# Performance work log

Measured on AMD Instinct MI355X. Metric: run time of the kernel, lower is better.

## Reference

```python
import jax, jax.numpy as jnp
import numpy as np
import math

ALPHA = 2.0  # spikingjelly surrogate.ATan default alpha
NB_STEPS, NUM_IN, NUM_HID, NUM_OUT = 100, 784, 100, 10
BATCH = 1024
TAU_LIF = 2.0

@jax.custom_vjp
def atan_spike(x):
    # Heaviside forward, ATan surrogate backward
    return (x >= 0.0).astype(x.dtype)

def _atan_fwd(x):
    return atan_spike(x), x

def _atan_bwd(x, g):
    return (g * (ALPHA / 2.0) / (1.0 + (jnp.pi / 2.0 * ALPHA * x) ** 2),)

atan_spike.defvjp(_atan_fwd, _atan_bwd)


def setup_inputs() -> dict:
    key = jax.random.key(0)
    ks = jax.random.split(key, 3)
    x = jax.random.normal(ks[0], (BATCH, NB_STEPS, NUM_IN), jnp.float32)
    tau_syn = 2.0
    # spikingjelly SynapseFilter(learnable=True): w init = -log(tau - 1)
    w_syn1 = jnp.asarray(-math.log(tau_syn - 1.0), jnp.float32)
    w_syn2 = jnp.asarray(-math.log(tau_syn - 1.0), jnp.float32)
    W1 = jax.random.normal(ks[1], (NUM_HID, NUM_IN), jnp.float32) / np.sqrt(NUM_IN).astype(np.float32)
    b1 = jnp.zeros((NUM_HID,), jnp.float32)
    W2 = jax.random.normal(ks[2], (NUM_OUT, NUM_HID), jnp.float32) / np.sqrt(NUM_HID).astype(np.float32)
    b2 = jnp.zeros((NUM_OUT,), jnp.float32)
    return dict(x=x, w_syn1=w_syn1, W1=W1, b1=b1, w_syn2=w_syn2, W2=W2, b2=b2)


def reference(x, w_syn1, W1, b1, w_syn2, W2, b2):
    B = x.shape[0]
    inv1 = jax.nn.sigmoid(w_syn1)  # 1/tau of filter 1
    inv2 = jax.nn.sigmoid(w_syn2)
    s1 = jnp.zeros((B, NUM_IN), x.dtype)
    v1 = jnp.zeros((B, NUM_HID), x.dtype)
    s2 = jnp.zeros((B, NUM_HID), x.dtype)
    v2 = jnp.zeros((B, NUM_OUT), x.dtype)

    def step(carry, xt):
        s1, v1, s2, v2 = carry
        # SynapseFilter 1: s = s - s*sigmoid(w) + in
        s1 = s1 - s1 * inv1 + xt
        h1 = s1 @ W1.T + b1
        # LIF 1: decay_input=True, v_reset=0: v += (x - (v - 0)) / tau
        v1 = v1 + (h1 - v1) / TAU_LIF
        sp1 = atan_spike(v1 - 1.0)       # v_threshold = 1.0
        v1 = v1 * (1.0 - sp1)            # hard reset to v_reset = 0
        # SynapseFilter 2
        s2 = s2 - s2 * inv2 + sp1
        h2 = s2 @ W2.T + b2
        # LIF 2: v_reset=None (soft reset), v_threshold=0, decay_input=True
        v2 = v2 + (h2 - v2) / TAU_LIF
        sp2 = atan_spike(v2 - 0.0)
        v2 = v2 - sp2 * 0.0              # soft reset subtracts spike*threshold (=0)
        return (s1, v1, s2, v2), None

    (s1, v1, s2, v2), _ = jax.lax.scan(step, (s1, v1, s2, v2), jnp.swapaxes(x, 0, 1))
    # Net.forward returns self.fc[-1].v: final membrane potential of last LIF
    return v2
```

## Files before the change

kernel.cpp:

```cpp
#include <hip/hip_runtime.h>
#include <math.h>


#define NSTEPS 100
#define NHID 100
#define KDIM 784
#define BK 16
#define NOUT 10

__global__ __launch_bounds__(256, 2)
void snn_fused2(const float* __restrict__ X, const float* __restrict__ wsyn1p,
                const float* __restrict__ W1, const float* __restrict__ b1,
                const float* __restrict__ wsyn2p, const float* __restrict__ W2,
                const float* __restrict__ b2, float* __restrict__ out) {
  __shared__ float Xs[BK][256];
  __shared__ float Ws[BK][112];
  __shared__ float Cs[2][25][106];
  __shared__ float zsh[2][NHID];

  const int tid = threadIdx.x;
  const int l   = tid & 63;
  const int cg  = __builtin_amdgcn_readfirstlane(tid >> 6);
  const long b0 = 2L * blockIdx.x;

  const int sb = tid >> 7;
  const int st = ((tid & 127) < NSTEPS) ? (tid & 127) : (NSTEPS - 1);
  const float* __restrict__ Xrow = X + ((b0 + sb) * NSTEPS + st) * (size_t)KDIM;
  const int wj0 = tid >> 2, wkq = tid & 3;
  const int g0 = wj0 / 25, c0 = wj0 % 25;
  const int wj1 = wj0 + 64;
  const int g1 = wj1 / 25, c1 = wj1 % 25;
  const float* __restrict__ Wp0 = W1 + (size_t)wj0 * KDIM + 4 * wkq;
  const float* __restrict__ Wp1 = W1 + (size_t)wj1 * KDIM + 4 * wkq;

  float acc[4][25];
#pragma unroll
  for (int i = 0; i < 4; ++i)
#pragma unroll
    for (int c = 0; c < 25; ++c) acc[i][c] = 0.0f;

  float4 xr0 = *(const float4*)(Xrow + 0);
  float4 xr1 = *(const float4*)(Xrow + 4);
  float4 xr2 = *(const float4*)(Xrow + 8);
  float4 xr3 = *(const float4*)(Xrow + 12);
  float4 wr0 = *(const float4*)(Wp0);
  float4 wr1 = (tid < 144) ? *(const float4*)(Wp1) : float4{0, 0, 0, 0};

  for (int kt = 0; kt < KDIM; kt += BK) {
    __syncthreads();
    Xs[0][tid] = xr0.x;  Xs[1][tid] = xr0.y;  Xs[2][tid] = xr0.z;  Xs[3][tid] = xr0.w;
    Xs[4][tid] = xr1.x;  Xs[5][tid] = xr1.y;  Xs[6][tid] = xr1.z;  Xs[7][tid] = xr1.w;
    Xs[8][tid] = xr2.x;  Xs[9][tid] = xr2.y;  Xs[10][tid] = xr2.z; Xs[11][tid] = xr2.w;
    Xs[12][tid] = xr3.x; Xs[13][tid] = xr3.y; Xs[14][tid] = xr3.z; Xs[15][tid] = xr3.w;
    {
      float* w = &Ws[4 * wkq][28 * g0 + c0];
      w[0] = wr0.x; w[112] = wr0.y; w[224] = wr0.z; w[336] = wr0.w;
    }
    if (tid < 144) {
      float* w = &Ws[4 * wkq][28 * g1 + c1];
      w[0] = wr1.x; w[112] = wr1.y; w[224] = wr1.z; w[336] = wr1.w;
    }
    __syncthreads();
    if (kt + BK < KDIM) {
      const float* xp = Xrow + kt + BK;
      xr0 = *(const float4*)(xp + 0);
      xr1 = *(const float4*)(xp + 4);
      xr2 = *(const float4*)(xp + 8);
      xr3 = *(const float4*)(xp + 12);
      wr0 = *(const float4*)(Wp0 + kt + BK);
      if (tid < 144) wr1 = *(const float4*)(Wp1 + kt + BK);
    }
#pragma unroll
    for (int k = 0; k < BK; ++k) {
      const float4 xv = *(const float4*)&Xs[k][4 * l];
      const float* __restrict__ wk = &Ws[k][28 * cg];
#pragma unroll
      for (int g = 0; g < 6; ++g) {
        const float4 wv = *(const float4*)(wk + 4 * g);
        acc[0][4*g+0] = fmaf(xv.x, wv.x, acc[0][4*g+0]);
        acc[1][4*g+0] = fmaf(xv.y, wv.x, acc[1][4*g+0]);
        acc[2][4*g+0] = fmaf(xv.z, wv.x, acc[2][4*g+0]);
        acc[3][4*g+0] = fmaf(xv.w, wv.x, acc[3][4*g+0]);
        acc[0][4*g+1] = fmaf(xv.x, wv.y, acc[0][4*g+1]);
        acc[1][4*g+1] = fmaf(xv.y, wv.y, acc[1][4*g+1]);
        acc[2][4*g+1] = fmaf(xv.z, wv.y, acc[2][4*g+1]);
        acc[3][4*g+1] = fmaf(xv.w, wv.y, acc[3][4*g+1]);
        acc[0][4*g+2] = fmaf(xv.x, wv.z, acc[0][4*g+2]);
        acc[1][4*g+2] = fmaf(xv.y, wv.z, acc[1][4*g+2]);
        acc[2][4*g+2] = fmaf(xv.z, wv.z, acc[2][4*g+2]);
        acc[3][4*g+2] = fmaf(xv.w, wv.z, acc[3][4*g+2]);
        acc[0][4*g+3] = fmaf(xv.x, wv.w, acc[0][4*g+3]);
        acc[1][4*g+3] = fmaf(xv.y, wv.w, acc[1][4*g+3]);
        acc[2][4*g+3] = fmaf(xv.z, wv.w, acc[2][4*g+3]);
        acc[3][4*g+3] = fmaf(xv.w, wv.w, acc[3][4*g+3]);
      }
      const float w24 = wk[24];
      acc[0][24] = fmaf(xv.x, w24, acc[0][24]);
      acc[1][24] = fmaf(xv.y, w24, acc[1][24]);
      acc[2][24] = fmaf(xv.z, w24, acc[2][24]);
      acc[3][24] = fmaf(xv.w, w24, acc[3][24]);
    }
  }

  const float inv1 = 1.f / (1.f + expf(-wsyn1p[0]));
  const float inv2 = 1.f / (1.f + expf(-wsyn2p[0]));
  const int sb2 = tid >> 7;
  const int j   = tid & 127;
  const float bj = (j < NHID) ? b1[j] : 0.f;
  float S = 0.f, v1 = 0.f, s2 = 0.f, z = 0.f;
  float at = 0x1p-100f;

  for (int q = 0; q < 4; ++q) {
    __syncthreads();
#pragma unroll
    for (int i = 0; i < 4; ++i) {
      const int r = 4 * l + i;
      const int bb = r >> 7;
      const int t  = r & 127;
      const int tt = t - 25 * q;
      if (t < NSTEPS && tt >= 0 && tt < 25) {
#pragma unroll
        for (int c = 0; c < 25; ++c) Cs[bb][tt][25 * cg + c] = acc[i][c];
      }
    }
    __syncthreads();
    if (j < NHID) {
#pragma unroll
      for (int tt = 0; tt < 25; ++tt) {
        const float u = Cs[sb2][tt][j];
        S = S - S * inv1 + u;
        const float h = S + bj;
        v1 = v1 + (h - v1) * 0.5f;
        const float sp = (v1 >= 1.0f) ? 1.0f : 0.0f;
        v1 = v1 * (1.0f - sp);
        s2 = s2 - s2 * inv2 + sp;
        z  = fmaf(at, s2, z);
        at *= 2.0f;
      }
    }
  }

  if (j < NHID) zsh[sb2][j] = z;
  __syncthreads();

  if (tid < 2 * NOUT) {
    const int bb = tid / NOUT;
    const int jo = tid % NOUT;
    float a = b2[jo];
    const float* __restrict__ wrow = W2 + jo * NHID;
#pragma unroll
    for (int jj = 0; jj < NHID; ++jj) a = fmaf(zsh[bb][jj], wrow[jj], a);
    out[(b0 + bb) * NOUT + jo] = a;
  }
}

extern "C" void kernel_launch(void* const* d_in, const int* in_sizes, int n_in,
                              void* d_out, int out_size, void* d_ws, size_t ws_size,
                              hipStream_t stream) {
  const float* x     = (const float*)d_in[0];
  const float* wsyn1 = (const float*)d_in[1];
  const float* W1    = (const float*)d_in[2];
  const float* b1    = (const float*)d_in[3];
  const float* wsyn2 = (const float*)d_in[4];
  const float* W2    = (const float*)d_in[5];
  const float* b2    = (const float*)d_in[6];
  float* out = (float*)d_out;

  snn_fused2<<<dim3(512), dim3(256), 0, stream>>>(x, wsyn1, W1, b1, wsyn2, W2,
                                                  b2, out);
}
```

Baseline: 561.7 us.

## Pre-transpose W1 to workspace and use packed FP32 FMAs with global W reads

Adds a small kernel that transposes W1 into a padded k-major layout in the workspace. The main kernel then stops staging W through LDS and instead has each wavefront read its 25-column W slice straight from global/L2 (uniform across lanes). The inner product switches to 2-wide packed FMAs (v_pk_fma_f32) and uses a larger K tile of 28. The goal is to cut LDS traffic and barriers and to double FMA throughput, at the cost of an extra kernel launch and many per-k global loads of W that depend on cache hits.

New measurement: 554.1 us. No clear change (-1.4%).

```diff
diff --git a/kernel.cpp b/kernel.cpp
--- a/kernel.cpp
+++ b/kernel.cpp
@@ -5,16 +5,26 @@
 #define NSTEPS 100
 #define NHID 100
 #define KDIM 784
-#define BK 16
+#define BKT 28
 #define NOUT 10
 
+typedef float v2f __attribute__((ext_vector_type(2)));
+
+__global__ __launch_bounds__(256)
+void wt_transpose(const float* __restrict__ W1, float* __restrict__ Wt) {
+  const int idx = blockIdx.x * 256 + threadIdx.x;
+  if (idx >= KDIM * 128) return;
+  const int k = idx >> 7, s = idx & 127, cg = s >> 5, i = s & 31;
+  const int j = 25 * cg + i;
+  Wt[idx] = (i < 25) ? W1[(size_t)j * KDIM + k] : 0.0f;
+}
+
 __global__ __launch_bounds__(256, 2)
-void snn_fused2(const float* __restrict__ X, const float* __restrict__ wsyn1p,
-                const float* __restrict__ W1, const float* __restrict__ b1,
+void snn_fused3(const float* __restrict__ X, const float* __restrict__ Wt,
+                const float* __restrict__ wsyn1p, const float* __restrict__ b1,
                 const float* __restrict__ wsyn2p, const float* __restrict__ W2,
                 const float* __restrict__ b2, float* __restrict__ out) {
-  __shared__ float Xs[BK][256];
-  __shared__ float Ws[BK][112];
+  __shared__ float Xs[BKT][256];
   __shared__ float Cs[2][25][106];
   __shared__ float zsh[2][NHID];
 
@@ -26,79 +36,64 @@
   const int sb = tid >> 7;
   const int st = ((tid & 127) < NSTEPS) ? (tid & 127) : (NSTEPS - 1);
   const float* __restrict__ Xrow = X + ((b0 + sb) * NSTEPS + st) * (size_t)KDIM;
-  const int wj0 = tid >> 2, wkq = tid & 3;
-  const int g0 = wj0 / 25, c0 = wj0 % 25;
-  const int wj1 = wj0 + 64;
-  const int g1 = wj1 / 25, c1 = wj1 % 25;
-  const float* __restrict__ Wp0 = W1 + (size_t)wj0 * KDIM + 4 * wkq;
-  const float* __restrict__ Wp1 = W1 + (size_t)wj1 * KDIM + 4 * wkq;
 
-  float acc[4][25];
+  v2f  acc2[4][12];
+  float accs[4];
 #pragma unroll
-  for (int i = 0; i < 4; ++i)
+  for (int i = 0; i < 4; ++i) {
+    accs[i] = 0.0f;
 #pragma unroll
-    for (int c = 0; c < 25; ++c) acc[i][c] = 0.0f;
+    for (int c = 0; c < 12; ++c) acc2[i][c] = (v2f){0.0f, 0.0f};
+  }
 
-  float4 xr0 = *(const float4*)(Xrow + 0);
-  float4 xr1 = *(const float4*)(Xrow + 4);
-  float4 xr2 = *(const float4*)(Xrow + 8);
-  float4 xr3 = *(const float4*)(Xrow + 12);
-  float4 wr0 = *(const float4*)(Wp0);
-  float4 wr1 = (tid < 144) ? *(const float4*)(Wp1) : float4{0, 0, 0, 0};
+  float4 pf[7];
+#pragma unroll
+  for (int q = 0; q < 7; ++q) pf[q] = *(const float4*)(Xrow + 4 * q);
 
-  for (int kt = 0; kt < KDIM; kt += BK) {
+  const float* __restrict__ wgrp = Wt + 32 * cg;
+
+  for (int kt = 0; kt < KDIM; kt += BKT) {
     __syncthreads();
-    Xs[0][tid] = xr0.x;  Xs[1][tid] = xr0.y;  Xs[2][tid] = xr0.z;  Xs[3][tid] = xr0.w;
-    Xs[4][tid] = xr1.x;  Xs[5][tid] = xr1.y;  Xs[6][tid] = xr1.z;  Xs[7][tid] = xr1.w;
-    Xs[8][tid] = xr2.x;  Xs[9][tid] = xr2.y;  Xs[10][tid] = xr2.z; Xs[11][tid] = xr2.w;
-    Xs[12][tid] = xr3.x; Xs[13][tid] = xr3.y; Xs[14][tid] = xr3.z; Xs[15][tid] = xr3.w;
-    {
-      float* w = &Ws[4 * wkq][28 * g0 + c0];
-      w[0] = wr0.x; w[112] = wr0.y; w[224] = wr0.z; w[336] = wr0.w;
-    }
-    if (tid < 144) {
-      float* w = &Ws[4 * wkq][28 * g1 + c1];
-      w[0] = wr1.x; w[112] = wr1.y; w[224] = wr1.z; w[336] = wr1.w;
+#pragma unroll
+    for (int q = 0; q < 7; ++q) {
+      Xs[4 * q + 0][tid] = pf[q].x;
+      Xs[4 * q + 1][tid] = pf[q].y;
+      Xs[4 * q + 2][tid] = pf[q].z;
+      Xs[4 * q + 3][tid] = pf[q].w;
     }
     __syncthreads();
-    if (kt + BK < KDIM) {
-      const float* xp = Xrow + kt + BK;
-      xr0 = *(const float4*)(xp + 0);
-      xr1 = *(const float4*)(xp + 4);
-      xr2 = *(const float4*)(xp + 8);
-      xr3 = *(const float4*)(xp + 12);
-      wr0 = *(const float4*)(Wp0 + kt + BK);
-      if (tid < 144) wr1 = *(const float4*)(Wp1 + kt + BK);
+    if (kt + BKT < KDIM) {
+      const float* xp = Xrow + kt + BKT;
+#pragma unroll
+      for (int q = 0; q < 7; ++q) pf[q] = *(const float4*)(xp + 4 * q);
     }
+
+#pragma unroll 4
+    for (int k = 0; k < BKT; ++k) {
+      const float4 xv = *(const float4*)&Xs[k][4 * l];
+      const float* __restrict__ wk = wgrp + (size_t)(kt + k) * 128;
+      float w[26];
 #pragma unroll
-    for (int k = 0; k < BK; ++k) {
-      const float4 xv = *(const float4*)&Xs[k][4 * l];
-      const float* __restrict__ wk = &Ws[k][28 * cg];
+      for (int i2 = 0; i2 < 13; ++i2)
+        *(v2f*)(w + 2 * i2) = *(const v2f*)(wk + 2 * i2);
+
+      const v2f xd0 = {xv.x, xv.x};
+      const v2f xd1 = {xv.y, xv.y};
+      const v2f xd2 = {xv.z, xv.z};
+      const v2f xd3 = {xv.w, xv.w};
 #pragma unroll
-      for (int g = 0; g < 6; ++g) {
-        const float4 wv = *(const float4*)(wk + 4 * g);
-        acc[0][4*g+0] = fmaf(xv.x, wv.x, acc[0][4*g+0]);
-        acc[1][4*g+0] = fmaf(xv.y, wv.x, acc[1][4*g+0]);
-        acc[2][4*g+0] = fmaf(xv.z, wv.x, acc[2][4*g+0]);
-        acc[3][4*g+0] = fmaf(xv.w, wv.x, acc[3][4*g+0]);
-        acc[0][4*g+1] = fmaf(xv.x, wv.y, acc[0][4*g+1]);
-        acc[1][4*g+1] = fmaf(xv.y, wv.y, acc[1][4*g+1]);
-        acc[2][4*g+1] = fmaf(xv.z, wv.y, acc[2][4*g+1]);
-        acc[3][4*g+1] = fmaf(xv.w, wv.y, acc[3][4*g+1]);
-        acc[0][4*g+2] = fmaf(xv.x, wv.z, acc[0][4*g+2]);
-        acc[1][4*g+2] = fmaf(xv.y, wv.z, acc[1][4*g+2]);
-        acc[2][4*g+2] = fmaf(xv.z, wv.z, acc[2][4*g+2]);
-        acc[3][4*g+2] = fmaf(xv.w, wv.z, acc[3][4*g+2]);
-        acc[0][4*g+3] = fmaf(xv.x, wv.w, acc[0][4*g+3]);
-        acc[1][4*g+3] = fmaf(xv.y, wv.w, acc[1][4*g+3]);
-        acc[2][4*g+3] = fmaf(xv.z, wv.w, acc[2][4*g+3]);
-        acc[3][4*g+3] = fmaf(xv.w, wv.w, acc[3][4*g+3]);
+      for (int c2 = 0; c2 < 12; ++c2) {
+        const v2f wv = *(const v2f*)(w + 2 * c2);
+        acc2[0][c2] = __builtin_elementwise_fma(xd0, wv, acc2[0][c2]);
+        acc2[1][c2] = __builtin_elementwise_fma(xd1, wv, acc2[1][c2]);
+        acc2[2][c2] = __builtin_elementwise_fma(xd2, wv, acc2[2][c2]);
+        acc2[3][c2] = __builtin_elementwise_fma(xd3, wv, acc2[3][c2]);
       }
-      const float w24 = wk[24];
-      acc[0][24] = fmaf(xv.x, w24, acc[0][24]);
-      acc[1][24] = fmaf(xv.y, w24, acc[1][24]);
-      acc[2][24] = fmaf(xv.z, w24, acc[2][24]);
-      acc[3][24] = fmaf(xv.w, w24, acc[3][24]);
+      const float w24 = w[24];
+      accs[0] = fmaf(xv.x, w24, accs[0]);
+      accs[1] = fmaf(xv.y, w24, accs[1]);
+      accs[2] = fmaf(xv.z, w24, accs[2]);
+      accs[3] = fmaf(xv.w, w24, accs[3]);
     }
   }
 
@@ -114,13 +109,18 @@
     __syncthreads();
 #pragma unroll
     for (int i = 0; i < 4; ++i) {
-      const int r = 4 * l + i;
+      const int r  = 4 * l + i;
       const int bb = r >> 7;
       const int t  = r & 127;
       const int tt = t - 25 * q;
       if (t < NSTEPS && tt >= 0 && tt < 25) {
+        float* crow = &Cs[bb][tt][25 * cg];
 #pragma unroll
-        for (int c = 0; c < 25; ++c) Cs[bb][tt][25 * cg + c] = acc[i][c];
+        for (int c2 = 0; c2 < 12; ++c2) {
+          crow[2 * c2 + 0] = acc2[i][c2].x;
+          crow[2 * c2 + 1] = acc2[i][c2].y;
+        }
+        crow[24] = accs[i];
       }
     }
     __syncthreads();
@@ -165,7 +165,9 @@
   const float* W2    = (const float*)d_in[5];
   const float* b2    = (const float*)d_in[6];
   float* out = (float*)d_out;
+  float* Wt  = (float*)d_ws;
 
-  snn_fused2<<<dim3(512), dim3(256), 0, stream>>>(x, wsyn1, W1, b1, wsyn2, W2,
+  wt_transpose<<<dim3((KDIM * 128 + 255) / 256), dim3(256), 0, stream>>>(W1, Wt);
+  snn_fused3<<<dim3(512), dim3(256), 0, stream>>>(x, Wt, wsyn1, b1, wsyn2, W2,
                                                   b2, out);
 }
```
